# Kernel optimization log

Hardware: AMD Instinct MI355X
Metric: run time of the kernel (lower is better)

Reference implementation:

```python
import jax, jax.numpy as jnp
import numpy as np


def _wn(W, g):
    # weight_norm with dim=None: scalar g times W / ||W||_F
    return (g / jnp.linalg.norm(W)) * W


def setup_inputs() -> dict:
    key = jax.random.key(0)
    ks = jax.random.split(key, 8)
    B, N, D = 16, 1024, 128
    v_dim = q_dim = 1024
    K = 1024 * 3  # h_dim * k
    h_out = 8
    s = 0.02
    return {
        "v": jax.random.normal(ks[0], (B, N, v_dim), jnp.float32),
        "q": jax.random.normal(ks[1], (B, D, q_dim), jnp.float32),
        "Wv": jax.random.normal(ks[2], (K, v_dim), jnp.float32) * s,
        "gv": jnp.ones((), jnp.float32),
        "bv": jax.random.normal(ks[3], (K,), jnp.float32) * s,
        "Wq": jax.random.normal(ks[4], (K, q_dim), jnp.float32) * s,
        "gq": jnp.ones((), jnp.float32),
        "bq": jax.random.normal(ks[5], (K,), jnp.float32) * s,
        "h_mat": jax.random.normal(ks[6], (1, h_out, 1, K), jnp.float32) * s,
        "h_bias": jnp.zeros((1, h_out, 1, 1), jnp.float32),
    }


def reference(v, q, Wv, gv, bv, Wq, gq, bq, h_mat, h_bias):
    # v_net / q_net: single weight-normed Linear (dropout inactive at inference)
    v_ = jnp.einsum('bnc,kc->bnk', v, _wn(Wv, gv)) + bv  # (B,N,K)
    q_ = jnp.einsum('bdc,kc->bdk', q, _wn(Wq, gq)) + bq  # (B,D,K)
    hm = h_mat[0, :, 0, :]                               # (H,K)
    # logits[b,h,n,d] = sum_k hm[h,k] * v_[b,n,k] * q_[b,d,k]
    logits = jnp.einsum('hk,bnk,bdk->bhnd', hm, v_, q_) + h_bias
    return logits
```

## Files before the change

### kernel.cpp

```cpp
#include <hip/hip_runtime.h>
#include <hip/hip_bf16.h>
#include <math.h>

typedef unsigned short u16;
typedef unsigned int u32;

typedef __bf16 bf16x8 __attribute__((ext_vector_type(8)));
typedef float f32x4 __attribute__((ext_vector_type(4)));

union U8 { uint4 u; u16 s[8]; };

__device__ __forceinline__ float b2f(u16 x) {
    u32 y = ((u32)x) << 16;
    return __builtin_bit_cast(float, y);
}
__device__ __forceinline__ u16 f2b(float f) {
    u32 x = __builtin_bit_cast(u32, f);
    u32 r = x + 0x7fffu + ((x >> 16) & 1u);
    return (u16)(r >> 16);
}
__device__ __forceinline__ uint4 cvt8(float4 a, float4 b) {
    U8 o;
    o.s[0] = f2b(a.x); o.s[1] = f2b(a.y); o.s[2] = f2b(a.z); o.s[3] = f2b(a.w);
    o.s[4] = f2b(b.x); o.s[5] = f2b(b.y); o.s[6] = f2b(b.z); o.s[7] = f2b(b.w);
    return o.u;
}

__device__ __forceinline__ void gload16(const u16* g, const u16* l) {
    __builtin_amdgcn_global_load_lds(
        (const __attribute__((address_space(1))) void*)g,
        (__attribute__((address_space(3))) void*)l, 16, 0, 0);
}


__global__ void __launch_bounds__(64) zero_ss(float* ss) {
    if (threadIdx.x < 2) ss[threadIdx.x] = 0.f;
}

__global__ void __launch_bounds__(256)
prep_k(const float* __restrict__ Wv, const float* __restrict__ Wq,
       const float* __restrict__ q, const float* __restrict__ v,
       const float* __restrict__ hm, float* __restrict__ ss,
       u16* __restrict__ wvh, u16* __restrict__ qb,
       u16* __restrict__ wqb, u16* __restrict__ vb) {
    const int bid = blockIdx.x, tid = threadIdx.x;
    if (bid < 3072) {
        __shared__ float t[32][33];
        int bx = bid & 31, by = bid >> 5;
        int cx0 = bx * 32, ky0 = by * 32;
        int tx = tid & 31, ty = tid >> 5;
#pragma unroll
        for (int j = ty; j < 32; j += 8)
            t[j][tx] = Wv[(size_t)(ky0 + j) * 1024 + cx0 + tx];
        __syncthreads();
        int k = ky0 + tx;
        float hv[8];
#pragma unroll
        for (int h = 0; h < 8; h++) hv[h] = hm[(size_t)h * 3072 + k];
#pragma unroll
        for (int j = ty; j < 32; j += 8) {
            float w = t[tx][j];
            int c = cx0 + j;
#pragma unroll
            for (int h = 0; h < 8; h++)
                wvh[(size_t)h * 3145728 + (size_t)c * 3072 + k] = f2b(hv[h] * w);
        }
    } else if (bid < 3584) {
        int sub = bid - 3072;
        const float* W = (sub < 256) ? Wv : Wq;
        int lb = sub & 255;
        float acc = 0.f;
        const size_t stride = (size_t)256 * 256 * 8;
        for (size_t i = ((size_t)lb * 256 + tid) * 8; i < (size_t)(3072 * 1024); i += stride) {
            float4 a = *(const float4*)(W + i);
            float4 b = *(const float4*)(W + i + 4);
            acc += a.x * a.x + a.y * a.y + a.z * a.z + a.w * a.w;
            acc += b.x * b.x + b.y * b.y + b.z * b.z + b.w * b.w;
        }
#pragma unroll
        for (int o = 32; o > 0; o >>= 1) acc += __shfl_down(acc, o, 64);
        __shared__ float red[4];
        int lane = tid & 63, w6 = tid >> 6;
        if (lane == 0) red[w6] = acc;
        __syncthreads();
        if (tid == 0) atomicAdd(&ss[sub >> 8], red[0] + red[1] + red[2] + red[3]);
    } else if (bid < 4608) {
        size_t i = ((size_t)(bid - 3584) * 256 + tid) * 8;
        float4 a = *(const float4*)(q + i);
        float4 b = *(const float4*)(q + i + 4);
        *(uint4*)(qb + i) = cvt8(a, b);
    } else if (bid < 6144) {
        size_t i = ((size_t)(bid - 4608) * 256 + tid) * 8;
        float4 a = *(const float4*)(Wq + i);
        float4 b = *(const float4*)(Wq + i + 4);
        *(uint4*)(wqb + i) = cvt8(a, b);
    } else {
        const size_t stride = (size_t)2048 * 256 * 8;
        for (size_t i = ((size_t)(bid - 6144) * 256 + tid) * 8; i < (size_t)16777216; i += stride) {
            float4 a = *(const float4*)(v + i);
            float4 b = *(const float4*)(v + i + 4);
            *(uint4*)(vb + i) = cvt8(a, b);
        }
    }
}

__global__ void __launch_bounds__(256) const_k(const u16* __restrict__ qbuf,
                                               const float* __restrict__ bv,
                                               const float* __restrict__ hm,
                                               float* __restrict__ cb) {
    int idx = blockIdx.x * 256 + threadIdx.x;
    int b = idx >> 10, hd = idx & 1023, h = hd >> 7, d = hd & 127;
    const u16* qr = qbuf + ((size_t)b * 128 + d) * 3072;
    const float* hr = hm + (size_t)h * 3072;
    float acc = 0.f;
    for (int k = 0; k < 3072; k += 8) {
        U8 uq; uq.u = *(const uint4*)(qr + k);
        float4 h0 = *(const float4*)(hr + k);
        float4 h1 = *(const float4*)(hr + k + 4);
        float4 b0 = *(const float4*)(bv + k);
        float4 b1 = *(const float4*)(bv + k + 4);
        acc += b2f(uq.s[0]) * h0.x * b0.x + b2f(uq.s[1]) * h0.y * b0.y +
               b2f(uq.s[2]) * h0.z * b0.z + b2f(uq.s[3]) * h0.w * b0.w +
               b2f(uq.s[4]) * h1.x * b1.x + b2f(uq.s[5]) * h1.y * b1.y +
               b2f(uq.s[6]) * h1.z * b1.z + b2f(uq.s[7]) * h1.w * b1.w;
    }
    cb[idx] = acc;
}

template <int EPI, bool A_BF16>
__global__ void __launch_bounds__(256)
gemm_bt(const void* __restrict__ Ap, const u16* __restrict__ Bp, void* __restrict__ C,
        const float* __restrict__ ss, int ss_idx, const float* __restrict__ g,
        const float* __restrict__ bias, const float* __restrict__ cb,
        const float* __restrict__ hbias, int kdim, size_t abatch, size_t bbatch) {
    constexpr int BK = 32;
    __shared__ __align__(16) u16 sA[2][128 * BK];
    __shared__ __align__(16) u16 sB[2][128 * BK];

    const int tid = threadIdx.x;
    const int lane = tid & 63, wv = tid >> 6;
    const int wm = (wv & 1) * 64, wn = (wv >> 1) * 64;
    const int lr = lane & 15, quad = lane >> 4;
    const int z = blockIdx.z;
    const int arow0 = blockIdx.y * 128;
    const int bcol0 = blockIdx.x * 128;

    const size_t aoff = (size_t)z * abatch;
    const size_t boff = (size_t)z * bbatch;

    const int srow = 16 * wv + (lane >> 2);
    const int qcg  = (lane & 3) ^ ((lane >> 3) & 3);
    const int lb0  = wv * 512;
    const int lb1  = lb0 + 2048;

    const u16* gB0 = Bp + boff + (size_t)(bcol0 + srow) * kdim + qcg * 8;
    const u16* gB1 = gB0 + (size_t)64 * kdim;

    const int r0 = tid >> 2, c0 = (tid & 3) * 8;
    const int w0 = r0 * 32 + (((tid & 3) ^ ((tid >> 3) & 3)) * 8);
    const int w1 = w0 + 2048;

    const u16* gA0 = nullptr; const u16* gA1 = nullptr;
    const float* fA0 = nullptr; const float* fA1 = nullptr;
    if constexpr (A_BF16) {
        gA0 = (const u16*)Ap + aoff + (size_t)(arow0 + srow) * kdim + qcg * 8;
        gA1 = gA0 + (size_t)64 * kdim;
    } else {
        fA0 = (const float*)Ap + aoff + (size_t)(arow0 + r0) * kdim + c0;
        fA1 = fA0 + (size_t)64 * kdim;
    }

    const int rsw = (quad ^ ((lr >> 1) & 3)) * 8;

    if constexpr (A_BF16) {
        gload16(gA0, sA[0] + lb0);
        gload16(gA1, sA[0] + lb1);
        gA0 += BK; gA1 += BK;
    } else {
        float4 x0 = *(const float4*)fA0, x1 = *(const float4*)(fA0 + 4);
        float4 y0 = *(const float4*)fA1, y1 = *(const float4*)(fA1 + 4);
        *(uint4*)(sA[0] + w0) = cvt8(x0, x1);
        *(uint4*)(sA[0] + w1) = cvt8(y0, y1);
        fA0 += BK; fA1 += BK;
    }
    gload16(gB0, sB[0] + lb0);
    gload16(gB1, sB[0] + lb1);
    gB0 += BK; gB1 += BK;

    f32x4 acc[4][4];
#pragma unroll
    for (int im = 0; im < 4; im++)
#pragma unroll
        for (int in = 0; in < 4; in++) acc[im][in] = (f32x4){0.f, 0.f, 0.f, 0.f};

    __syncthreads();

    int p = 0;
    for (int kt = 0; kt < kdim; kt += BK) {
        const bool more = (kt + BK < kdim);

        float4 ax0, ax1, ay0, ay1;
        if (more) {
            if constexpr (A_BF16) {
                gload16(gA0, sA[p ^ 1] + lb0);
                gload16(gA1, sA[p ^ 1] + lb1);
                gA0 += BK; gA1 += BK;
            } else {
                ax0 = *(const float4*)fA0; ax1 = *(const float4*)(fA0 + 4);
                ay0 = *(const float4*)fA1; ay1 = *(const float4*)(fA1 + 4);
                fA0 += BK; fA1 += BK;
            }
            gload16(gB0, sB[p ^ 1] + lb0);
            gload16(gB1, sB[p ^ 1] + lb1);
            gB0 += BK; gB1 += BK;
        }

        const u16* sAp = sA[p];
        const u16* sBp = sB[p];
        bf16x8 af[4], bfr[4];
#pragma unroll
        for (int im = 0; im < 4; im++)
            af[im] = *(const bf16x8*)(sAp + (wm + im * 16 + lr) * 32 + rsw);
#pragma unroll
        for (int in = 0; in < 4; in++)
            bfr[in] = *(const bf16x8*)(sBp + (wn + in * 16 + lr) * 32 + rsw);
#pragma unroll
        for (int im = 0; im < 4; im++)
#pragma unroll
            for (int in = 0; in < 4; in++)
                acc[im][in] = __builtin_amdgcn_mfma_f32_16x16x32_bf16(af[im], bfr[in], acc[im][in], 0, 0, 0);

        if (more) {
            if constexpr (!A_BF16) {
                u16* dA = sA[p ^ 1];
                *(uint4*)(dA + w0) = cvt8(ax0, ax1);
                *(uint4*)(dA + w1) = cvt8(ay0, ay1);
            }
        }
        __syncthreads();
        p ^= 1;
    }

    float scale = 1.f;
    if constexpr (EPI == 0 || EPI == 2) scale = g[0] / sqrtf(ss[ss_idx]);

#pragma unroll
    for (int im = 0; im < 4; im++) {
#pragma unroll
        for (int in = 0; in < 4; in++) {
#pragma unroll
            for (int reg = 0; reg < 4; reg++) {
                int gr = arow0 + wm + im * 16 + quad * 4 + reg;
                int gc = bcol0 + wn + in * 16 + lr;
                float val = acc[im][in][reg];
                if constexpr (EPI == 0) {
                    ((u16*)C)[(size_t)gr * 3072 + gc] = f2b(val * scale + bias[gc]);
                } else if constexpr (EPI == 1) {
                    size_t idx = (((size_t)(gr >> 7) * 8 + (gc >> 10)) * 128 + (gr & 127)) * 1024
                               + (gc & 1023);
                    ((u16*)C)[idx] = f2b(val);
                } else {
                    int h = gc >> 7, d = gc & 127;
                    float o = val * scale + cb[(size_t)z * 1024 + gc] + hbias[h];
                    ((float*)C)[(((size_t)z * 8 + h) * 1024 + gr) * 128 + d] = o;
                }
            }
        }
    }
}

template <int EPI>
__global__ void __launch_bounds__(512, 2)
gemm8p(const u16* __restrict__ Ap, const u16* __restrict__ Bp, void* __restrict__ C,
       const float* __restrict__ ss, const float* __restrict__ g,
       const float* __restrict__ cb, const float* __restrict__ hbias,
       int kdim, size_t abatch, size_t bbatch) {
    __shared__ __align__(16) u16 sAb[2][256 * 64];
    __shared__ __align__(16) u16 sBb[2][256 * 64];

    const int tid = threadIdx.x;
    const int lane = tid & 63, wv = tid >> 6;
    const int wm = (wv & 1) * 128;
    const int wn = (wv >> 1) * 64;
    const int lr = lane & 15, quad = lane >> 4;
    const int z = blockIdx.z;

    int bx, by;
    if constexpr (EPI == 1) {
        int orig = blockIdx.y * 32 + blockIdx.x;
        int xcd = orig & 7, idx = orig >> 3;
        bx = (xcd << 2) | (idx & 3);
        by = idx >> 2;
    } else {
        bx = blockIdx.x; by = blockIdx.y;
    }
    const int arow0 = by * 256, bcol0 = bx * 256;

    const size_t aoff = (size_t)z * abatch, boff = (size_t)z * bbatch;

    const int sg = (tid & 7) ^ ((tid >> 3) & 7);
    const u16* gA = Ap + aoff + (size_t)(arow0 + (tid >> 3)) * kdim + sg * 8;
    const u16* gB = Bp + boff + (size_t)(bcol0 + (tid >> 3)) * kdim + sg * 8;
    const size_t ldk64 = (size_t)64 * kdim;
    const int ldst = wv * 512;

    const int slot = (quad ^ (lane & 7)) * 8;
    const int rbA = (wm + lr) * 64 + slot;
    const int rbB = (wn + lr) * 64 + slot;

    f32x4 acc[8][4];
#pragma unroll
    for (int im = 0; im < 8; im++)
#pragma unroll
        for (int in = 0; in < 4; in++) acc[im][in] = (f32x4){0.f, 0.f, 0.f, 0.f};

    gload16(gB + 0 * ldk64, sBb[0] + 0 * 4096 + ldst);
    gload16(gB + 1 * ldk64, sBb[0] + 1 * 4096 + ldst);
    gload16(gB + 2 * ldk64, sBb[0] + 2 * 4096 + ldst);
    gload16(gB + 3 * ldk64, sBb[0] + 3 * 4096 + ldst);
    gload16(gA + 0 * ldk64, sAb[0] + 0 * 4096 + ldst);
    gload16(gA + 1 * ldk64, sAb[0] + 1 * 4096 + ldst);
    gload16(gA + 2 * ldk64, sAb[0] + 2 * 4096 + ldst);
    gload16(gA + 3 * ldk64, sAb[0] + 3 * 4096 + ldst);
    gA += 64; gB += 64;
    asm volatile("s_waitcnt vmcnt(0)" ::: "memory");
    __builtin_amdgcn_s_barrier();

    const u16* sAd = sAb[0];
    const u16* sBd = sBb[0];
    u16* dA = (u16*)sAb[1];
    u16* dB = (u16*)sBb[1];

    bf16x8 af[4], bfr[4], af1[4], af2[4], bf2[4], af3[4];
#pragma unroll
    for (int n = 0; n < 4; n++) bfr[n] = *(const bf16x8*)(sBd + rbB + n * 1024);
#pragma unroll
    for (int j = 0; j < 4; j++) af[j] = *(const bf16x8*)(sAd + rbA + j * 1024);

    const int NT = kdim >> 6;
    for (int t = 0; t < NT; ++t) {
        const bool stg = (t + 1 < NT);

        if (stg) {
            gload16(gB + 0 * ldk64, dB + 0 * 4096 + ldst);
            gload16(gB + 1 * ldk64, dB + 1 * 4096 + ldst);
            gload16(gB + 2 * ldk64, dB + 2 * 4096 + ldst);
            gload16(gB + 3 * ldk64, dB + 3 * 4096 + ldst);
            gload16(gA + 0 * ldk64, dA + 0 * 4096 + ldst);
            gload16(gA + 1 * ldk64, dA + 1 * 4096 + ldst);
            gload16(gA + 2 * ldk64, dA + 2 * 4096 + ldst);
            gload16(gA + 3 * ldk64, dA + 3 * 4096 + ldst);
        }

#pragma unroll
        for (int j = 0; j < 4; j++) af1[j] = *(const bf16x8*)(sAd + rbA + (4 + j) * 1024);
        __builtin_amdgcn_s_setprio(1);
#pragma unroll
        for (int j = 0; j < 4; j++)
#pragma unroll
            for (int n = 0; n < 4; n++)
                acc[j][n] = __builtin_amdgcn_mfma_f32_16x16x32_bf16(af[j], bfr[n], acc[j][n], 0, 0, 0);
        __builtin_amdgcn_s_setprio(0);

#pragma unroll
        for (int n = 0; n < 4; n++) bf2[n] = *(const bf16x8*)(sBd + (rbB ^ 32) + n * 1024);
#pragma unroll
        for (int j = 0; j < 4; j++) af2[j] = *(const bf16x8*)(sAd + (rbA ^ 32) + j * 1024);
        __builtin_amdgcn_s_setprio(1);
#pragma unroll
        for (int j = 0; j < 4; j++)
#pragma unroll
            for (int n = 0; n < 4; n++)
                acc[4 + j][n] = __builtin_amdgcn_mfma_f32_16x16x32_bf16(af1[j], bfr[n], acc[4 + j][n], 0, 0, 0);
        __builtin_amdgcn_s_setprio(0);

#pragma unroll
        for (int j = 0; j < 4; j++) af3[j] = *(const bf16x8*)(sAd + (rbA ^ 32) + (4 + j) * 1024);
        __builtin_amdgcn_s_setprio(1);
#pragma unroll
        for (int j = 0; j < 4; j++)
#pragma unroll
            for (int n = 0; n < 4; n++)
                acc[j][n] = __builtin_amdgcn_mfma_f32_16x16x32_bf16(af2[j], bf2[n], acc[j][n], 0, 0, 0);
        __builtin_amdgcn_s_setprio(0);

        asm volatile("s_waitcnt vmcnt(0)" ::: "memory");
        asm volatile("s_waitcnt lgkmcnt(0)" ::: "memory");
        __builtin_amdgcn_s_barrier();

        if (stg) {
#pragma unroll
            for (int n = 0; n < 4; n++) bfr[n] = *(const bf16x8*)(dB + rbB + n * 1024);
#pragma unroll
            for (int j = 0; j < 4; j++) af[j] = *(const bf16x8*)(dA + rbA + j * 1024);
        }
        __builtin_amdgcn_s_setprio(1);
#pragma unroll
        for (int j = 0; j < 4; j++)
#pragma unroll
            for (int n = 0; n < 4; n++)
                acc[4 + j][n] = __builtin_amdgcn_mfma_f32_16x16x32_bf16(af3[j], bf2[n], acc[4 + j][n], 0, 0, 0);
        __builtin_amdgcn_s_setprio(0);

        const u16* tp = sAd; sAd = dA; dA = (u16*)tp;
        tp = sBd; sBd = dB; dB = (u16*)tp;
        gA += 64; gB += 64;
    }

    float scale = 1.f;
    if constexpr (EPI == 2) scale = g[0] / sqrtf(ss[0]);

#pragma unroll
    for (int im = 0; im < 8; im++) {
#pragma unroll
        for (int in = 0; in < 4; in++) {
#pragma unroll
            for (int reg = 0; reg < 4; reg++) {
                int gr = arow0 + wm + im * 16 + quad * 4 + reg;
                int gc = bcol0 + wn + in * 16 + lr;
                float val = acc[im][in][reg];
                if constexpr (EPI == 1) {
                    size_t idx = (((size_t)(gr >> 7) * 8 + (gc >> 10)) * 128 + (gr & 127)) * 1024
                               + (gc & 1023);
                    ((u16*)C)[idx] = f2b(val);
                } else {
                    int h = gc >> 7, d = gc & 127;
                    float o = val * scale + cb[(size_t)z * 1024 + gc] + hbias[h];
                    ((float*)C)[(((size_t)z * 8 + h) * 1024 + gr) * 128 + d] = o;
                }
            }
        }
    }
}


extern "C" void kernel_launch(void* const* d_in, const int* in_sizes, int n_in,
                              void* d_out, int out_size, void* d_ws, size_t ws_size,
                              hipStream_t stream) {
    (void)in_sizes; (void)n_in; (void)out_size;
    const float* v  = (const float*)d_in[0];
    const float* q  = (const float*)d_in[1];
    const float* Wv = (const float*)d_in[2];
    const float* gv = (const float*)d_in[3];
    const float* bv = (const float*)d_in[4];
    const float* Wq = (const float*)d_in[5];
    const float* gq = (const float*)d_in[6];
    const float* bq = (const float*)d_in[7];
    const float* hm = (const float*)d_in[8];
    const float* hb = (const float*)d_in[9];
    float* out = (float*)d_out;

    char* ws = (char*)d_ws;
    float* ss   = (float*)ws;
    float* cb   = (float*)(ws + 256);
    u16*   qbuf = (u16*)(ws + 256 + 65536);
    u16*   tbuf = (u16*)(ws + 256 + 65536 + 12582912);
    u16*   vb   = (u16*)(ws + 256 + 65536 + 12582912 + 33554432);
    const size_t need_vb = 256 + 65536 + 12582912 + 33554432 + 33554432;
    const bool fullfat = (ws_size >= need_vb);

    u16* wvh = (u16*)d_out;
    u16* qb  = (u16*)((char*)d_out + 50331648);
    u16* wqb = (u16*)((char*)d_out + 54525952);

    zero_ss<<<1, 64, 0, stream>>>(ss);

    prep_k<<<fullfat ? 8192 : 6144, 256, 0, stream>>>(
        Wv, Wq, q, v, hm, ss, wvh, qb, wqb, vb);

    gemm_bt<0, true><<<dim3(24, 16, 1), 256, 0, stream>>>(
        qb, wqb, qbuf, ss, 1, gq, bq, nullptr, nullptr, 1024, 0, 0);

    const_k<<<64, 256, 0, stream>>>(qbuf, bv, hm, cb);

    gemm8p<1><<<dim3(32, 8, 1), 512, 0, stream>>>(
        qbuf, wvh, tbuf, nullptr, nullptr, nullptr, nullptr, 3072, 0, 0);

    if (fullfat) {
        gemm8p<2><<<dim3(4, 4, 16), 512, 0, stream>>>(
            vb, tbuf, out, ss, gv, cb, hb, 1024, 1048576, 1048576);
    } else {
        gemm_bt<2, false><<<dim3(8, 8, 16), 256, 0, stream>>>(
            v, tbuf, out, ss, 0, gv, nullptr, cb, hb, 1024, 1048576, 1048576);
    }
}
```

Measured before the change: 385.9 us.

## Split const_k reduction across lanes and remap GEMM blocks for XCD locality

const_k now gives each output four threads, each covering a quarter of K, and combines the partials with shuffles. The kernel launches 256 blocks instead of 64, which fills far more CUs for this small reduction. gemm_bt (EPI 0) and gemm8p (EPI 2) also remap block indices so blocks placed on the same XCD share A/B tiles or the same batch, aiming for better L2 reuse. The remaps add a little index arithmetic and assume the fixed grid shapes.

After: 366.2 us. -5.1%, faster.

```diff
diff --git a/kernel.cpp b/kernel.cpp
--- a/kernel.cpp
+++ b/kernel.cpp
@@ -108,23 +108,27 @@
                                                const float* __restrict__ bv,
                                                const float* __restrict__ hm,
                                                float* __restrict__ cb) {
-    int idx = blockIdx.x * 256 + threadIdx.x;
-    int b = idx >> 10, hd = idx & 1023, h = hd >> 7, d = hd & 127;
-    const u16* qr = qbuf + ((size_t)b * 128 + d) * 3072;
-    const float* hr = hm + (size_t)h * 3072;
+    int o = blockIdx.x * 64 + (threadIdx.x >> 2);
+    int qt = threadIdx.x & 3;
+    int b = o >> 10, hd = o & 1023, h = hd >> 7, d = hd & 127;
+    const u16* qr = qbuf + ((size_t)b * 128 + d) * 3072 + qt * 768;
+    const float* hr = hm + (size_t)h * 3072 + qt * 768;
+    const float* br = bv + qt * 768;
     float acc = 0.f;
-    for (int k = 0; k < 3072; k += 8) {
+    for (int k = 0; k < 768; k += 8) {
         U8 uq; uq.u = *(const uint4*)(qr + k);
         float4 h0 = *(const float4*)(hr + k);
         float4 h1 = *(const float4*)(hr + k + 4);
-        float4 b0 = *(const float4*)(bv + k);
-        float4 b1 = *(const float4*)(bv + k + 4);
+        float4 b0 = *(const float4*)(br + k);
+        float4 b1 = *(const float4*)(br + k + 4);
         acc += b2f(uq.s[0]) * h0.x * b0.x + b2f(uq.s[1]) * h0.y * b0.y +
                b2f(uq.s[2]) * h0.z * b0.z + b2f(uq.s[3]) * h0.w * b0.w +
                b2f(uq.s[4]) * h1.x * b1.x + b2f(uq.s[5]) * h1.y * b1.y +
                b2f(uq.s[6]) * h1.z * b1.z + b2f(uq.s[7]) * h1.w * b1.w;
     }
-    cb[idx] = acc;
+    acc += __shfl_xor(acc, 1, 64);
+    acc += __shfl_xor(acc, 2, 64);
+    if (qt == 0) cb[o] = acc;
 }
 
 template <int EPI, bool A_BF16>
@@ -142,8 +146,18 @@
     const int wm = (wv & 1) * 64, wn = (wv >> 1) * 64;
     const int lr = lane & 15, quad = lane >> 4;
     const int z = blockIdx.z;
-    const int arow0 = blockIdx.y * 128;
-    const int bcol0 = blockIdx.x * 128;
+
+    int bxx, byy;
+    if constexpr (EPI == 0) {
+        int lin = blockIdx.y * 24 + blockIdx.x;
+        int xcd = lin & 7, i = lin >> 3;
+        bxx = (xcd & 3) * 6 + i % 6;
+        byy = (xcd >> 2) * 8 + i / 6;
+    } else {
+        bxx = blockIdx.x; byy = blockIdx.y;
+    }
+    const int arow0 = byy * 128;
+    const int bcol0 = bxx * 128;
 
     const size_t aoff = (size_t)z * abatch;
     const size_t boff = (size_t)z * bbatch;
@@ -283,16 +297,20 @@
     const int wm = (wv & 1) * 128;
     const int wn = (wv >> 1) * 64;
     const int lr = lane & 15, quad = lane >> 4;
-    const int z = blockIdx.z;
-
-    int bx, by;
+
+    int bx, by, z;
     if constexpr (EPI == 1) {
         int orig = blockIdx.y * 32 + blockIdx.x;
         int xcd = orig & 7, idx = orig >> 3;
         bx = (xcd << 2) | (idx & 3);
         by = idx >> 2;
+        z = 0;
     } else {
-        bx = blockIdx.x; by = blockIdx.y;
+        int lin = (blockIdx.z * 4 + blockIdx.y) * 4 + blockIdx.x;
+        int xcd = lin & 7, i = lin >> 3;
+        z = xcd + 8 * (i >> 4);
+        int sub = i & 15;
+        bx = sub & 3; by = sub >> 2;
     }
     const int arow0 = by * 256, bcol0 = bx * 256;
 
@@ -471,7 +489,7 @@
     gemm_bt<0, true><<<dim3(24, 16, 1), 256, 0, stream>>>(
         qb, wqb, qbuf, ss, 1, gq, bq, nullptr, nullptr, 1024, 0, 0);
 
-    const_k<<<64, 256, 0, stream>>>(qbuf, bv, hm, cb);
+    const_k<<<256, 256, 0, stream>>>(qbuf, bv, hm, cb);
 
     gemm8p<1><<<dim3(32, 8, 1), 512, 0, stream>>>(
         qbuf, wvh, tbuf, nullptr, nullptr, nullptr, nullptr, 3072, 0, 0);
```
